# Performance work log

Measured on AMD Instinct MI355X. Metric: run time of the kernel, lower is better.

Reference implementation:

```python
import jax, jax.numpy as jnp
import numpy as np

P = 16            # decode steps == n_process
M = 4             # number of physical nodes
CAPACITY = [4, 4, 4, 4]
B = 4096          # batch
S = 16            # n_process (sequence length)
G = 128           # gnn_dim
E = 256           # n_embed
H = 512           # n_hidden
CLIP = 10.0       # clip_logits
MASK_PENALTY = 1e8


def setup_inputs() -> dict:
    key = jax.random.key(0)
    ks = jax.random.split(key, 16)
    u = lambda k, shape: jax.random.uniform(k, shape, jnp.float32, -0.08, 0.08)
    return {
        "x": jax.random.normal(ks[0], (B, S, G), jnp.float32),
        "emb_W": u(ks[1], (E, G)),                 # embedding Linear (no bias)
        "enc_Wih": u(ks[2], (4 * H, E)),           # encoder LSTM (gate order i,f,g,o)
        "enc_Whh": u(ks[3], (4 * H, H)),
        "enc_b": u(ks[4], (4 * H,)),               # b_ih + b_hh folded into one bias
        "dec_Wih": u(ks[5], (4 * H, E)),           # decoder LSTM
        "dec_Whh": u(ks[6], (4 * H, H)),
        "dec_b": u(ks[7], (4 * H,)),
        "Wq2": u(ks[8], (H, H)),                   # pointer W_q2
        "bq2": u(ks[9], (H,)),
        "Wref2": u(ks[10], (H, H)),                # pointer W_ref2 (conv1d k=1 == linear)
        "bref2": u(ks[11], (H,)),
        "Vec2": u(ks[12], (H,)),
        "dec_input0": u(ks[13], (E,)),             # learned initial decoder input
    }


def lstm_cell(x, h, c, Wih, Whh, b):
    g = x @ Wih.T + h @ Whh.T + b
    i, f, gg, o = jnp.split(g, 4, axis=-1)
    c = jax.nn.sigmoid(f) * c + jax.nn.sigmoid(i) * jnp.tanh(gg)
    h = jax.nn.sigmoid(o) * jnp.tanh(c)
    return h, c


def reference(x, emb_W, enc_Wih, enc_Whh, enc_b, dec_Wih, dec_Whh, dec_b,
              Wq2, bq2, Wref2, bref2, Vec2, dec_input0):
    Bx, Sx, _ = x.shape
    emb = x @ emb_W.T                                  # (B,S,E)

    # ---- encoder LSTM over the sequence ----
    def enc_step(carry, xt):
        h, c = carry
        h, c = lstm_cell(xt, h, c, enc_Wih, enc_Whh, enc_b)
        return (h, c), h

    h0 = jnp.zeros((Bx, H), emb.dtype)
    (h, c), enc_hs = jax.lax.scan(enc_step, (h0, h0), jnp.swapaxes(emb, 0, 1))
    ref = jnp.swapaxes(enc_hs, 0, 1)                   # (B,S,H)

    # W_ref2 conv1d(k=1) applied to ref is step-invariant: hoist out of the loop
    u2 = jnp.einsum('bsh,oh->bso', ref, Wref2) + bref2  # (B,S,H)

    dec0 = jnp.broadcast_to(dec_input0, (Bx, E))
    mask0 = jnp.zeros((Bx, Sx), emb.dtype)

    def dec_step(carry, _):
        h, c, din, mask = carry
        h, c = lstm_cell(din, h, c, dec_Wih, dec_Whh, dec_b)
        qp = h @ Wq2.T + bq2                           # (B,H)
        t = CLIP * jnp.tanh(qp[:, None, :] + u2)       # (B,S,H)
        logits = jnp.einsum('h,bsh->bs', Vec2, t) - MASK_PENALTY * mask
        log_p = jax.nn.log_softmax(logits, axis=-1)    # (B,S)
        nxt = jnp.argmax(log_p, axis=1)                # greedy node selector
        din = jnp.take_along_axis(emb, nxt[:, None, None], axis=1)[:, 0, :]
        mask = mask + jax.nn.one_hot(nxt, Sx, dtype=mask.dtype)
        return (h, c, din, mask), (nxt, log_p)

    _, (pis, log_ps) = jax.lax.scan(dec_step, (h, c, dec0, mask0), None, length=P)
    pi = jnp.swapaxes(pis, 0, 1)                       # (B,P)
    log_ps = jnp.swapaxes(log_ps, 0, 1)                # (B,P,S)

    # log-likelihood of the chosen tour
    ll = jnp.take_along_axis(log_ps, pi[:, :, None], axis=2)[..., 0].sum(axis=1)

    # __get_mapping: node id per step depends only on the capacity vector
    nodes = jnp.asarray(np.repeat(np.arange(M), np.asarray(CAPACITY))[:P], jnp.int32)
    rows = jnp.arange(Bx)
    mapping = jnp.full((Bx, P), -1, jnp.int32)
    mapping = mapping.at[rows[:, None], pi].set(jnp.broadcast_to(nodes, (Bx, P)))
    return mapping, ll
```

## Files before the change

### kernel.cpp

```cpp
#include <hip/hip_runtime.h>
#include <cstddef>

#define Bsz  4096
#define Sseq 16
#define Gdim 128
#define Edim 256
#define Hdim 512
#define H4   2048
#define Psteps 16
#define BK   16

typedef short bfrag8 __attribute__((ext_vector_type(8)));
typedef float f32x4  __attribute__((ext_vector_type(4)));

__device__ __forceinline__ void split3(float f, unsigned short& h,
                                       unsigned short& m, unsigned short& l) {
    unsigned u = __float_as_uint(f);
    h = (unsigned short)(u >> 16);
    float r1 = f - __uint_as_float(u & 0xffff0000u);
    unsigned u1 = __float_as_uint(r1);
    m = (unsigned short)(u1 >> 16);
    float r2 = r1 - __uint_as_float(u1 & 0xffff0000u);
    l = (unsigned short)(__float_as_uint(r2) >> 16);
}

__global__ void fold_kernel(const float* __restrict__ encWih,
                            const float* __restrict__ encWhh,
                            const float* __restrict__ enc_b,
                            const float* __restrict__ decWih,
                            const float* __restrict__ decWhh,
                            const float* __restrict__ dec_b,
                            const float* __restrict__ embW,
                            const float* __restrict__ dec0,
                            unsigned short* __restrict__ encEh,
                            unsigned short* __restrict__ encEm,
                            unsigned short* __restrict__ encEl,
                            unsigned short* __restrict__ encWh,
                            unsigned short* __restrict__ encWm,
                            unsigned short* __restrict__ encWl,
                            unsigned short* __restrict__ decEh,
                            unsigned short* __restrict__ decEm,
                            unsigned short* __restrict__ decEl,
                            unsigned short* __restrict__ decWh,
                            unsigned short* __restrict__ decWm,
                            unsigned short* __restrict__ decWl,
                            float* __restrict__ encBI, float* __restrict__ decBI,
                            float* __restrict__ v0bI) {
    const int o = blockIdx.x;
    const int gate = o >> 9, j = o & 511;
    const int c = j * 4 + gate;
    const int g = threadIdx.x;
    float se = 0.f, sd = 0.f;
    for (int e = 0; e < Edim; ++e) {
        float w = embW[e * Gdim + g];
        se += encWih[(size_t)o * Edim + e] * w;
        sd += decWih[(size_t)o * Edim + e] * w;
    }
    unsigned short h, m, l;
    split3(se, h, m, l);
    encEh[(size_t)c * Gdim + g] = h; encEm[(size_t)c * Gdim + g] = m;
    encEl[(size_t)c * Gdim + g] = l;
    split3(sd, h, m, l);
    decEh[(size_t)c * Gdim + g] = h; decEm[(size_t)c * Gdim + g] = m;
    decEl[(size_t)c * Gdim + g] = l;
    for (int k = g; k < Hdim; k += Gdim) {
        split3(encWhh[(size_t)o * Hdim + k], h, m, l);
        encWh[(size_t)c * Hdim + k] = h; encWm[(size_t)c * Hdim + k] = m;
        encWl[(size_t)c * Hdim + k] = l;
        split3(decWhh[(size_t)o * Hdim + k], h, m, l);
        decWh[(size_t)c * Hdim + k] = h; decWm[(size_t)c * Hdim + k] = m;
        decWl[(size_t)c * Hdim + k] = l;
    }
    if (g == 0) {
        encBI[c] = enc_b[o];
        decBI[c] = dec_b[o];
        float s = dec_b[o];
        for (int e = 0; e < Edim; ++e) s += decWih[(size_t)o * Edim + e] * dec0[e];
        v0bI[c] = s;
    }
}

__global__ __launch_bounds__(256) void gates_mfma(
    const unsigned short* __restrict__ Wh1, const unsigned short* __restrict__ Wm1,
    const unsigned short* __restrict__ Wl1, int K1,
    const float* __restrict__ X, int ldx,
    const int* __restrict__ gather, int gmul,
    const unsigned short* __restrict__ Wh2, const unsigned short* __restrict__ Wm2,
    const unsigned short* __restrict__ Wl2, int K2,
    const float* __restrict__ Hin,
    const float* __restrict__ biasI,
    const float* __restrict__ c_in, float* __restrict__ h_out,
    float* __restrict__ c_out, int czero)
{
    __shared__ __align__(16) unsigned short wlds[2][3 * 4096];
    __shared__ __align__(16) float alds[2][128 * 32];

    const int tid = threadIdx.x;
    const int wv = tid >> 6, lane = tid & 63;
    const int wm = wv & 1, wn = wv >> 1;
    const int lm = lane & 15, quad = lane >> 4;
    const int c0 = blockIdx.y * 128;
    const int nT = c0 + wn * 64;
    const int mB0 = blockIdx.x * 128;

    int mrow[4];
#pragma unroll
    for (int tm = 0; tm < 4; ++tm) mrow[tm] = mB0 + wm * 64 + tm * 16 + lm;

    int srow[2], sqs[2];
#pragma unroll
    for (int i = 0; i < 2; ++i) {
        const int seg = i * 4 + wv;
        const int r = seg * 16 + (lane >> 2);
        srow[i] = r;
        sqs[i] = (lane & 3) ^ ((r >> 1) & 3);
    }
    size_t roff1[2], roff2[2];
#pragma unroll
    for (int i = 0; i < 2; ++i) {
        roff1[i] = (size_t)(c0 + srow[i]) * K1 + (size_t)(sqs[i] * 8);
        roff2[i] = (size_t)(c0 + srow[i]) * K2 + (size_t)(sqs[i] * 8);
    }

    const float* asrcX[4];
    const float* asrcH[4];
#pragma unroll
    for (int i = 0; i < 4; ++i) {
        const int r = (wv * 4 + i) * 8 + (lane >> 3);
        const int u = lane & 7;
        const int sw = (((u >> 1) ^ (r & 3)) << 3) + (u & 1) * 4;
        const int m = mB0 + r;
        if (X) {
            size_t off = (size_t)m * ldx;
            if (gather) off += (size_t)gather[m] * gmul;
            asrcX[i] = X + off + sw;
        }
        if (Hin) asrcH[i] = Hin + (size_t)m * K2 + sw;
    }

    int boffW[4];
#pragma unroll
    for (int tn = 0; tn < 4; ++tn) {
        const int r = wn * 64 + tn * 16 + lm;
        boffW[tn] = r * 32 + ((quad ^ ((r >> 1) & 3)) * 8);
    }
    int boffA[4];
#pragma unroll
    for (int tm = 0; tm < 4; ++tm) {
        const int r = wm * 64 + tm * 16 + lm;
        boffA[tm] = r * 32 + ((quad ^ (r & 3)) << 3);
    }

    auto stage = [&](int kcN, int buf) {
        const bool nX = kcN < K1;
        const int kb = nX ? kcN : kcN - K1;
#pragma unroll
        for (int i = 0; i < 2; ++i) {
            const int seg = i * 4 + wv;
            unsigned short* lb = &wlds[buf][seg * 512];
            const unsigned short* gh = (nX ? Wh1 + roff1[i] : Wh2 + roff2[i]) + kb;
            const unsigned short* gm = (nX ? Wm1 + roff1[i] : Wm2 + roff2[i]) + kb;
            const unsigned short* gl = (nX ? Wl1 + roff1[i] : Wl2 + roff2[i]) + kb;
            __builtin_amdgcn_global_load_lds(
                (const __attribute__((address_space(1))) void*)gh,
                (__attribute__((address_space(3))) void*)(lb), 16, 0, 0);
            __builtin_amdgcn_global_load_lds(
                (const __attribute__((address_space(1))) void*)gm,
                (__attribute__((address_space(3))) void*)(lb + 4096), 16, 0, 0);
            __builtin_amdgcn_global_load_lds(
                (const __attribute__((address_space(1))) void*)gl,
                (__attribute__((address_space(3))) void*)(lb + 8192), 16, 0, 0);
        }
#pragma unroll
        for (int i = 0; i < 4; ++i) {
            float* lb = &alds[buf][(wv * 4 + i) * 256];
            const float* src = (nX ? asrcX[i] : asrcH[i]) + kb;
            __builtin_amdgcn_global_load_lds(
                (const __attribute__((address_space(1))) void*)src,
                (__attribute__((address_space(3))) void*)lb, 16, 0, 0);
        }
    };

    f32x4 acc[4][4];
#pragma unroll
    for (int i = 0; i < 4; ++i)
#pragma unroll
        for (int j = 0; j < 4; ++j) acc[i][j] = (f32x4){0.f, 0.f, 0.f, 0.f};

    const int KT = K1 + K2;
    stage(0, 0);
    int cur = 0;

    for (int kc = 0; kc < KT; kc += 32) {
        __syncthreads();
        if (kc + 32 < KT) stage(kc + 32, cur ^ 1);

        const unsigned short* bufp = wlds[cur];
        bfrag8 ah[4], am4[4], al[4];
#pragma unroll
        for (int tn = 0; tn < 4; ++tn) {
            ah[tn]  = *(const bfrag8*)(bufp + boffW[tn]);
            am4[tn] = *(const bfrag8*)(bufp + 4096 + boffW[tn]);
            al[tn]  = *(const bfrag8*)(bufp + 8192 + boffW[tn]);
        }

        const float* abuf = alds[cur];
#pragma unroll
        for (int tm = 0; tm < 4; ++tm) {
            float a8[8];
            *(float4*)&a8[0] = *(const float4*)(abuf + boffA[tm]);
            *(float4*)&a8[4] = *(const float4*)(abuf + boffA[tm] + 4);
            bfrag8 bh, bm, bl;
#pragma unroll
            for (int j = 0; j < 8; ++j) {
                unsigned short h, m, l;
                split3(a8[j], h, m, l);
                bh[j] = (short)h; bm[j] = (short)m; bl[j] = (short)l;
            }
#pragma unroll
            for (int tn = 0; tn < 4; ++tn) {
                f32x4 c = acc[tn][tm];
                c = __builtin_amdgcn_mfma_f32_16x16x32_bf16(ah[tn], bl, c, 0, 0, 0);
                c = __builtin_amdgcn_mfma_f32_16x16x32_bf16(al[tn], bh, c, 0, 0, 0);
                c = __builtin_amdgcn_mfma_f32_16x16x32_bf16(am4[tn], bm, c, 0, 0, 0);
                c = __builtin_amdgcn_mfma_f32_16x16x32_bf16(ah[tn], bm, c, 0, 0, 0);
                c = __builtin_amdgcn_mfma_f32_16x16x32_bf16(am4[tn], bh, c, 0, 0, 0);
                c = __builtin_amdgcn_mfma_f32_16x16x32_bf16(ah[tn], bh, c, 0, 0, 0);
                acc[tn][tm] = c;
            }
        }
        cur ^= 1;
    }

#pragma unroll
    for (int tn = 0; tn < 4; ++tn) {
        const int nb = nT + tn * 16 + quad * 4;
        float4 bb = *(const float4*)(biasI + nb);
        const int j = nb >> 2;
#pragma unroll
        for (int tm = 0; tm < 4; ++tm) {
            const size_t idx = (size_t)mrow[tm] * Hdim + j;
            float gi = acc[tn][tm][0] + bb.x;
            float gf = acc[tn][tm][1] + bb.y;
            float gg = acc[tn][tm][2] + bb.z;
            float go = acc[tn][tm][3] + bb.w;
            float si = 1.f / (1.f + expf(-gi));
            float sf = 1.f / (1.f + expf(-gf));
            float so = 1.f / (1.f + expf(-go));
            float co = czero ? 0.f : c_in[idx];
            float cn = si * tanhf(gg) + sf * co;
            c_out[idx] = cn;
            h_out[idx] = so * tanhf(cn);
        }
    }
}

__global__ __launch_bounds__(256, 4) void gemm_sm(const float* __restrict__ A,
                                                  const float* __restrict__ W,
                                                  const float* __restrict__ bias,
                                                  float* __restrict__ C, int ldc)
{
    __shared__ float As[BK][64];
    __shared__ float Bs[BK][64];
    const int tid = threadIdx.x;
    const int rowBase = blockIdx.y * 64;
    const int colBase = blockIdx.x * 64;
    const int wv = tid >> 6;
    const int waveX = wv & 1, waveY = wv >> 1;
    const int lane = tid & 63;
    const int lx = lane & 7, ly = lane >> 3;
    const int rOff = waveY * 32 + ly * 4;
    const int cOff = waveX * 32 + lx * 4;

    const int ra = tid & 63;
    const int ka = (tid >> 6) * 4;
    const float* arow = A + (size_t)(rowBase + ra) * Hdim + ka;
    const float* brow = W + (size_t)(colBase + ra) * Hdim + ka;

    float4 aR, bR;
    float acc[4][4];
#pragma unroll
    for (int i = 0; i < 4; ++i)
#pragma unroll
        for (int j = 0; j < 4; ++j) acc[i][j] = 0.f;

    aR = *(const float4*)(arow);
    bR = *(const float4*)(brow);
    for (int kt = 0; kt < Hdim; kt += BK) {
        __syncthreads();
        As[ka + 0][ra] = aR.x; As[ka + 1][ra] = aR.y;
        As[ka + 2][ra] = aR.z; As[ka + 3][ra] = aR.w;
        Bs[ka + 0][ra] = bR.x; Bs[ka + 1][ra] = bR.y;
        Bs[ka + 2][ra] = bR.z; Bs[ka + 3][ra] = bR.w;
        __syncthreads();
        if (kt + BK < Hdim) {
            aR = *(const float4*)(arow + kt + BK);
            bR = *(const float4*)(brow + kt + BK);
        }
#pragma unroll
        for (int kk = 0; kk < BK; ++kk) {
            float4 av = *(const float4*)&As[kk][rOff];
            float4 bv = *(const float4*)&Bs[kk][cOff];
            const float* ap = (const float*)&av;
            const float* bp = (const float*)&bv;
#pragma unroll
            for (int i = 0; i < 4; ++i)
#pragma unroll
                for (int j = 0; j < 4; ++j) acc[i][j] += ap[i] * bp[j];
        }
    }

    float4 bb = *(const float4*)(bias + colBase + cOff);
#pragma unroll
    for (int i = 0; i < 4; ++i) {
        const int row = rowBase + rOff + i;
        float4 o;
        o.x = acc[i][0] + bb.x;
        o.y = acc[i][1] + bb.y;
        o.z = acc[i][2] + bb.z;
        o.w = acc[i][3] + bb.w;
        *(float4*)(C + (size_t)row * ldc + colBase + cOff) = o;
    }
}

__global__ __launch_bounds__(256) void attn_step(const float* __restrict__ qp,
                                                 const float* __restrict__ u2,
                                                 const float* __restrict__ Vec2,
                                                 float* __restrict__ mask,
                                                 float* __restrict__ ll_ws,
                                                 int* __restrict__ nxt,
                                                 float* __restrict__ out_map,
                                                 float* __restrict__ out_ll,
                                                 int step, int node) {
    const int b = blockIdx.x;
    __shared__ float qpS[Hdim];
    __shared__ float vS[Hdim];
    __shared__ float logitS[Sseq];
    const int tid = threadIdx.x;
    qpS[tid]       = qp[(size_t)b * Hdim + tid];
    qpS[tid + 256] = qp[(size_t)b * Hdim + 256 + tid];
    vS[tid]        = Vec2[tid];
    vS[tid + 256]  = Vec2[256 + tid];
    __syncthreads();

    const int wave = tid >> 6, lane = tid & 63;
    for (int si = 0; si < 4; ++si) {
        int s = wave * 4 + si;
        const float* u2p = u2 + ((size_t)b * Sseq + s) * Hdim;
        float sum = 0.f;
#pragma unroll
        for (int i = 0; i < 8; ++i) {
            int hh = lane + i * 64;
            sum += vS[hh] * tanhf(qpS[hh] + u2p[hh]);
        }
        for (int off = 32; off > 0; off >>= 1) sum += __shfl_down(sum, off);
        if (lane == 0) {
            float pen = step ? mask[b * Sseq + s] * 1e8f : 0.f;
            logitS[s] = 10.f * sum - pen;
        }
    }
    __syncthreads();

    if (tid == 0) {
        float mx = logitS[0];
        int am = 0;
        for (int s = 1; s < Sseq; ++s)
            if (logitS[s] > mx) { mx = logitS[s]; am = s; }
        float se = 0.f;
        for (int s = 0; s < Sseq; ++s) se += expf(logitS[s] - mx);
        float lp = -logf(se);
        float llv = (step ? ll_ws[b] : 0.f) + lp;
        ll_ws[b] = llv;
        out_ll[b] = llv;
        nxt[b] = am;
        if (step == 0) {
            for (int s = 0; s < Sseq; ++s) mask[b * Sseq + s] = (s == am) ? 1.f : 0.f;
        } else {
            mask[b * Sseq + am] += 1.f;
        }
        out_map[b * Sseq + am] = (float)node;
    }
}

extern "C" void kernel_launch(void* const* d_in, const int* in_sizes, int n_in,
                              void* d_out, int out_size, void* d_ws, size_t ws_size,
                              hipStream_t stream) {
    const float* x       = (const float*)d_in[0];
    const float* emb_W   = (const float*)d_in[1];
    const float* enc_Wih = (const float*)d_in[2];
    const float* enc_Whh = (const float*)d_in[3];
    const float* enc_b   = (const float*)d_in[4];
    const float* dec_Wih = (const float*)d_in[5];
    const float* dec_Whh = (const float*)d_in[6];
    const float* dec_b   = (const float*)d_in[7];
    const float* Wq2     = (const float*)d_in[8];
    const float* bq2     = (const float*)d_in[9];
    const float* Wref2   = (const float*)d_in[10];
    const float* bref2   = (const float*)d_in[11];
    const float* Vec2    = (const float*)d_in[12];
    const float* dec0    = (const float*)d_in[13];

    float* ws      = (float*)d_ws;
    float* u2      = ws;
    float* h0      = u2 + (size_t)Bsz * Sseq * Hdim;
    float* c0      = h0 + (size_t)Bsz * Hdim;
    float* h1      = c0 + (size_t)Bsz * Hdim;
    float* c1      = h1 + (size_t)Bsz * Hdim;
    float* qp      = c1 + (size_t)Bsz * Hdim;
    float* mask    = qp + (size_t)Bsz * Hdim;
    float* ll      = mask + (size_t)Bsz * Sseq;
    int*   nxt     = (int*)(ll + Bsz);
    float* encBI   = (float*)(nxt + Bsz);
    float* decBI   = encBI + H4;
    float* v0bI    = decBI + H4;
    unsigned short* us = (unsigned short*)(v0bI + H4);
    unsigned short* encEh = us;                       us += (size_t)H4 * Gdim;
    unsigned short* encEm = us;                       us += (size_t)H4 * Gdim;
    unsigned short* encEl = us;                       us += (size_t)H4 * Gdim;
    unsigned short* encWh = us;                       us += (size_t)H4 * Hdim;
    unsigned short* encWm = us;                       us += (size_t)H4 * Hdim;
    unsigned short* encWl = us;                       us += (size_t)H4 * Hdim;
    unsigned short* decEh = us;                       us += (size_t)H4 * Gdim;
    unsigned short* decEm = us;                       us += (size_t)H4 * Gdim;
    unsigned short* decEl = us;                       us += (size_t)H4 * Gdim;
    unsigned short* decWh = us;                       us += (size_t)H4 * Hdim;
    unsigned short* decWm = us;                       us += (size_t)H4 * Hdim;
    unsigned short* decWl = us;                       us += (size_t)H4 * Hdim;

    float* out_map = (float*)d_out;
    float* out_ll  = out_map + (size_t)Bsz * Psteps;

    static const int nodes[Psteps] = {0,0,0,0, 1,1,1,1, 2,2,2,2, 3,3,3,3};

    fold_kernel<<<H4, Gdim, 0, stream>>>(enc_Wih, enc_Whh, enc_b,
                                         dec_Wih, dec_Whh, dec_b,
                                         emb_W, dec0,
                                         encEh, encEm, encEl, encWh, encWm, encWl,
                                         decEh, decEm, decEl, decWh, decWm, decWl,
                                         encBI, decBI, v0bI);

    const dim3 gBig(32, 16);
    const dim3 gSm(8, 64);

    for (int t = 0; t < Sseq; ++t) {
        float* ho = (t & 1) ? h0 : h1;
        float* co = (t & 1) ? c0 : c1;
        const float* hi = (t & 1) ? h1 : h0;
        const float* ci = (t & 1) ? c1 : c0;
        if (t == 0) {
            gates_mfma<<<gBig, 256, 0, stream>>>(
                encEh, encEm, encEl, Gdim,
                x, Sseq * Gdim, nullptr, 0,
                nullptr, nullptr, nullptr, 0, nullptr,
                encBI, ci, ho, co, 1);
        } else {
            gates_mfma<<<gBig, 256, 0, stream>>>(
                encEh, encEm, encEl, Gdim,
                x + t * Gdim, Sseq * Gdim, nullptr, 0,
                encWh, encWm, encWl, Hdim, hi,
                encBI, ci, ho, co, 0);
        }
        gemm_sm<<<gSm, 256, 0, stream>>>(ho, Wref2, bref2,
                                         u2 + (size_t)t * Hdim, Sseq * Hdim);
    }

    for (int p = 0; p < Psteps; ++p) {
        const int u = Sseq + p;
        float* ho = (u & 1) ? h0 : h1;
        float* co = (u & 1) ? c0 : c1;
        const float* hi = (u & 1) ? h1 : h0;
        const float* ci = (u & 1) ? c1 : c0;
        if (p == 0) {
            gates_mfma<<<gBig, 256, 0, stream>>>(
                nullptr, nullptr, nullptr, 0,
                nullptr, 0, nullptr, 0,
                decWh, decWm, decWl, Hdim, hi,
                v0bI, ci, ho, co, 0);
        } else {
            gates_mfma<<<gBig, 256, 0, stream>>>(
                decEh, decEm, decEl, Gdim,
                x, Sseq * Gdim, nxt, Gdim,
                decWh, decWm, decWl, Hdim, hi,
                decBI, ci, ho, co, 0);
        }
        gemm_sm<<<gSm, 256, 0, stream>>>(ho, Wq2, bq2, qp, Hdim);
        attn_step<<<Bsz, 256, 0, stream>>>(qp, u2, Vec2, mask, ll, nxt,
                                           out_map, out_ll, p, nodes[p]);
    }
}
```

Baseline: 3.831 ms.

## Remap gates_mfma warps to 32x128 tiles so activation split is done once

Changes the per-warp tile in the LSTM gates MFMA kernel from a 2x2 warp grid (64 rows x 64 cols each) to four warps each owning 32 rows across all 128 columns. Each warp now splits only its own activation rows into bf16 hi/mid/lo. Before, the row split was duplicated across the two warps sharing each row range. The LDS swizzle for the fp32 activation tile is also changed to a new XOR pattern with separate half-fragment offsets. In exchange, weight fragments are read from LDS by every warp for all 128 columns, which doubles weight LDS reads per warp. Register pressure stays similar (8x2 accumulators).

```diff
diff --git a/kernel.cpp b/kernel.cpp
--- a/kernel.cpp
+++ b/kernel.cpp
@@ -97,15 +97,13 @@
 
     const int tid = threadIdx.x;
     const int wv = tid >> 6, lane = tid & 63;
-    const int wm = wv & 1, wn = wv >> 1;
     const int lm = lane & 15, quad = lane >> 4;
     const int c0 = blockIdx.y * 128;
-    const int nT = c0 + wn * 64;
     const int mB0 = blockIdx.x * 128;
 
-    int mrow[4];
-#pragma unroll
-    for (int tm = 0; tm < 4; ++tm) mrow[tm] = mB0 + wm * 64 + tm * 16 + lm;
+    int mrow[2];
+#pragma unroll
+    for (int tm = 0; tm < 2; ++tm) mrow[tm] = mB0 + wv * 32 + tm * 16 + lm;
 
     int srow[2], sqs[2];
 #pragma unroll
@@ -122,33 +120,33 @@
         roff2[i] = (size_t)(c0 + srow[i]) * K2 + (size_t)(sqs[i] * 8);
     }
 
+    const int asw = ((lane & 7) ^ (lane >> 3)) * 4;
     const float* asrcX[4];
     const float* asrcH[4];
 #pragma unroll
     for (int i = 0; i < 4; ++i) {
         const int r = (wv * 4 + i) * 8 + (lane >> 3);
-        const int u = lane & 7;
-        const int sw = (((u >> 1) ^ (r & 3)) << 3) + (u & 1) * 4;
         const int m = mB0 + r;
         if (X) {
             size_t off = (size_t)m * ldx;
             if (gather) off += (size_t)gather[m] * gmul;
-            asrcX[i] = X + off + sw;
-        }
-        if (Hin) asrcH[i] = Hin + (size_t)m * K2 + sw;
-    }
-
-    int boffW[4];
-#pragma unroll
-    for (int tn = 0; tn < 4; ++tn) {
-        const int r = wn * 64 + tn * 16 + lm;
+            asrcX[i] = X + off + asw;
+        }
+        if (Hin) asrcH[i] = Hin + (size_t)m * K2 + asw;
+    }
+
+    int boffW[8];
+#pragma unroll
+    for (int tn = 0; tn < 8; ++tn) {
+        const int r = tn * 16 + lm;
         boffW[tn] = r * 32 + ((quad ^ ((r >> 1) & 3)) * 8);
     }
-    int boffA[4];
-#pragma unroll
-    for (int tm = 0; tm < 4; ++tm) {
-        const int r = wm * 64 + tm * 16 + lm;
-        boffA[tm] = r * 32 + ((quad ^ (r & 3)) << 3);
+    int boffA1[2], boffA2[2];
+#pragma unroll
+    for (int tm = 0; tm < 2; ++tm) {
+        const int r = wv * 32 + tm * 16 + lm;
+        boffA1[tm] = r * 32 + (((2 * quad)     ^ (lm & 7)) << 2);
+        boffA2[tm] = r * 32 + (((2 * quad + 1) ^ (lm & 7)) << 2);
     }
 
     auto stage = [&](int kcN, int buf) {
@@ -181,11 +179,11 @@
         }
     };
 
-    f32x4 acc[4][4];
-#pragma unroll
-    for (int i = 0; i < 4; ++i)
-#pragma unroll
-        for (int j = 0; j < 4; ++j) acc[i][j] = (f32x4){0.f, 0.f, 0.f, 0.f};
+    f32x4 acc[8][2];
+#pragma unroll
+    for (int i = 0; i < 8; ++i)
+#pragma unroll
+        for (int j = 0; j < 2; ++j) acc[i][j] = (f32x4){0.f, 0.f, 0.f, 0.f};
 
     const int KT = K1 + K2;
     stage(0, 0);
@@ -195,50 +193,58 @@
         __syncthreads();
         if (kc + 32 < KT) stage(kc + 32, cur ^ 1);
 
-        const unsigned short* bufp = wlds[cur];
-        bfrag8 ah[4], am4[4], al[4];
-#pragma unroll
-        for (int tn = 0; tn < 4; ++tn) {
-            ah[tn]  = *(const bfrag8*)(bufp + boffW[tn]);
-            am4[tn] = *(const bfrag8*)(bufp + 4096 + boffW[tn]);
-            al[tn]  = *(const bfrag8*)(bufp + 8192 + boffW[tn]);
-        }
-
         const float* abuf = alds[cur];
-#pragma unroll
-        for (int tm = 0; tm < 4; ++tm) {
+        bfrag8 bh[2], bm[2], bl[2];
+#pragma unroll
+        for (int tm = 0; tm < 2; ++tm) {
             float a8[8];
-            *(float4*)&a8[0] = *(const float4*)(abuf + boffA[tm]);
-            *(float4*)&a8[4] = *(const float4*)(abuf + boffA[tm] + 4);
-            bfrag8 bh, bm, bl;
+            *(float4*)&a8[0] = *(const float4*)(abuf + boffA1[tm]);
+            *(float4*)&a8[4] = *(const float4*)(abuf + boffA2[tm]);
 #pragma unroll
             for (int j = 0; j < 8; ++j) {
                 unsigned short h, m, l;
                 split3(a8[j], h, m, l);
-                bh[j] = (short)h; bm[j] = (short)m; bl[j] = (short)l;
+                bh[tm][j] = (short)h; bm[tm][j] = (short)m; bl[tm][j] = (short)l;
             }
-#pragma unroll
-            for (int tn = 0; tn < 4; ++tn) {
-                f32x4 c = acc[tn][tm];
-                c = __builtin_amdgcn_mfma_f32_16x16x32_bf16(ah[tn], bl, c, 0, 0, 0);
-                c = __builtin_amdgcn_mfma_f32_16x16x32_bf16(al[tn], bh, c, 0, 0, 0);
-                c = __builtin_amdgcn_mfma_f32_16x16x32_bf16(am4[tn], bm, c, 0, 0, 0);
-                c = __builtin_amdgcn_mfma_f32_16x16x32_bf16(ah[tn], bm, c, 0, 0, 0);
-                c = __builtin_amdgcn_mfma_f32_16x16x32_bf16(am4[tn], bh, c, 0, 0, 0);
-                c = __builtin_amdgcn_mfma_f32_16x16x32_bf16(ah[tn], bh, c, 0, 0, 0);
-                acc[tn][tm] = c;
+        }
+
+        const unsigned short* bufp = wlds[cur];
+#pragma unroll
+        for (int hh = 0; hh < 2; ++hh) {
+            bfrag8 ah[4], am4[4], al[4];
+#pragma unroll
+            for (int t = 0; t < 4; ++t) {
+                const int tn = hh * 4 + t;
+                ah[t]  = *(const bfrag8*)(bufp + boffW[tn]);
+                am4[t] = *(const bfrag8*)(bufp + 4096 + boffW[tn]);
+                al[t]  = *(const bfrag8*)(bufp + 8192 + boffW[tn]);
             }
+#pragma unroll
+            for (int tm = 0; tm < 2; ++tm) {
+#pragma unroll
+                for (int t = 0; t < 4; ++t) {
+                    const int tn = hh * 4 + t;
+                    f32x4 c = acc[tn][tm];
+                    c = __builtin_amdgcn_mfma_f32_16x16x32_bf16(ah[t], bl[tm], c, 0, 0, 0);
+                    c = __builtin_amdgcn_mfma_f32_16x16x32_bf16(al[t], bh[tm], c, 0, 0, 0);
+                    c = __builtin_amdgcn_mfma_f32_16x16x32_bf16(am4[t], bm[tm], c, 0, 0, 0);
+                    c = __builtin_amdgcn_mfma_f32_16x16x32_bf16(ah[t], bm[tm], c, 0, 0, 0);
+                    c = __builtin_amdgcn_mfma_f32_16x16x32_bf16(am4[t], bh[tm], c, 0, 0, 0);
+                    c = __builtin_amdgcn_mfma_f32_16x16x32_bf16(ah[t], bh[tm], c, 0, 0, 0);
+                    acc[tn][tm] = c;
+                }
+            }
         }
         cur ^= 1;
     }
 
 #pragma unroll
-    for (int tn = 0; tn < 4; ++tn) {
-        const int nb = nT + tn * 16 + quad * 4;
+    for (int tn = 0; tn < 8; ++tn) {
+        const int nb = c0 + tn * 16 + quad * 4;
         float4 bb = *(const float4*)(biasI + nb);
         const int j = nb >> 2;
 #pragma unroll
-        for (int tm = 0; tm < 4; ++tm) {
+        for (int tm = 0; tm < 2; ++tm) {
             const size_t idx = (size_t)mrow[tm] * Hdim + j;
             float gi = acc[tn][tm][0] + bb.x;
             float gf = acc[tn][tm][1] + bb.y;
```

Result: no change. 3.862 ms (+0.8%).
